# Kernel optimization log

Measured on AMD Instinct MI355X. Metric: run time of the kernel, lower is better.

## Reference

```python
import jax, jax.numpy as jnp
import numpy as np

B, S, D, H = 4, 2048, 1024, 16
DEPTH = D // H


def setup_inputs() -> dict:
    key = jax.random.key(0)
    ks = jax.random.split(key, 11)
    s = 1.0 / np.sqrt(D)
    return {
        "q": jax.random.normal(ks[0], (B, S, D), jnp.float32),
        "k": jax.random.normal(ks[1], (B, S, D), jnp.float32),
        "v": jax.random.normal(ks[2], (B, S, D), jnp.float32),
        "wq": jax.random.normal(ks[3], (D, D), jnp.float32) * s,
        "bq": jnp.zeros((D,), jnp.float32),
        "wk": jax.random.normal(ks[4], (D, D), jnp.float32) * s,
        "bk": jnp.zeros((D,), jnp.float32),
        "wv": jax.random.normal(ks[5], (D, D), jnp.float32) * s,
        "bv": jnp.zeros((D,), jnp.float32),
        "wo": jax.random.normal(ks[6], (D, D), jnp.float32) * s,
        "bo": jnp.zeros((D,), jnp.float32),
    }


def _split_heads(x):
    # [B,S,D] -> [B,H,S,depth]
    b, s, _ = x.shape
    return x.reshape(b, s, H, DEPTH).transpose(0, 2, 1, 3)


def reference(q, k, v, wq, bq, wk, bk, wv, bv, wo, bo):
    qh = _split_heads(q @ wq + bq)
    kh = _split_heads(k @ wk + bk)
    vh = _split_heads(v @ wv + bv)
    scale = 1.0 / jnp.sqrt(jnp.asarray(DEPTH, jnp.float32))
    logits = jnp.einsum("bhsd,bhtd->bhst", qh, kh) * scale  # [B,H,S,S]
    attn = jax.nn.softmax(logits, axis=-1)
    out = jnp.einsum("bhst,bhtd->bhsd", attn, vh)
    out = out.transpose(0, 2, 1, 3).reshape(q.shape[0], -1, D)
    return out @ wo + bo
```

## Files before the change

kernel.cpp:

```cpp
#include <hip/hip_runtime.h>
#include <hip/hip_bf16.h>

#define BATCH 4
#define SEQ   2048
#define DIM   1024
#define NHEAD 16
#define HDIM  64

typedef __bf16    bf16x8 __attribute__((ext_vector_type(8)));
typedef float     f32x16 __attribute__((ext_vector_type(16)));
typedef unsigned  u32;

__device__ __forceinline__ unsigned short f2bfu(float x) {
  union { __hip_bfloat16 b; unsigned short u; } c; c.b = __float2bfloat16(x); return c.u;
}
__device__ __forceinline__ u32 cvtpk(float lo, float hi) {
  u32 r; asm("v_cvt_pk_bf16_f32 %0, %1, %2" : "=v"(r) : "v"(lo), "v"(hi)); return r;
}
__device__ __forceinline__ int swz4(int row) {
  return ((row & 7) ^ ((row >> 3) & 7)) << 2;
}

#define GLDS16(GP, LP)                                                         \
  __builtin_amdgcn_global_load_lds(                                            \
      (const __attribute__((address_space(1))) void*)(GP),                     \
      (__attribute__((address_space(3))) void*)(LP), 16, 0, 0)

__global__ __launch_bounds__(256)
void wtrans(const float* __restrict__ w0, const float* __restrict__ w1,
            const float* __restrict__ w2,
            __hip_bfloat16* __restrict__ t0, __hip_bfloat16* __restrict__ t1,
            __hip_bfloat16* __restrict__ t2)
{
  __shared__ float T[64][68];
  const int mat  = blockIdx.x >> 8;
  const int tile = blockIdx.x & 255;
  const float* W = mat == 0 ? w0 : (mat == 1 ? w1 : w2);
  __hip_bfloat16* Wt = mat == 0 ? t0 : (mat == 1 ? t1 : t2);
  const int k0 = (tile >> 4) * 64, n0 = (tile & 15) * 64;
  const int tid = threadIdx.x;
  const int r = tid >> 2, cq = (tid & 3) * 16;
  #pragma unroll
  for (int j = 0; j < 4; ++j) {
    const float4 v = *reinterpret_cast<const float4*>(&W[(size_t)(k0 + r) * DIM + n0 + cq + j * 4]);
    T[r][cq + j * 4 + 0] = v.x; T[r][cq + j * 4 + 1] = v.y;
    T[r][cq + j * 4 + 2] = v.z; T[r][cq + j * 4 + 3] = v.w;
  }
  __syncthreads();
  u32 o[8];
  #pragma unroll
  for (int j = 0; j < 8; ++j)
    o[j] = cvtpk(T[cq + 2 * j][r], T[cq + 2 * j + 1][r]);
  *reinterpret_cast<uint4*>(&Wt[(size_t)(n0 + r) * DIM + k0 + cq + 0]) = make_uint4(o[0], o[1], o[2], o[3]);
  *reinterpret_cast<uint4*>(&Wt[(size_t)(n0 + r) * DIM + k0 + cq + 8]) = make_uint4(o[4], o[5], o[6], o[7]);
}

template<typename TIN, typename TOUT, int NSEG>
__global__ __launch_bounds__(256, 2)
void gemm1ph(const TIN* __restrict__ A0, const TIN* __restrict__ A1, const TIN* __restrict__ A2,
             const __hip_bfloat16* __restrict__ W0, const __hip_bfloat16* __restrict__ W1,
             const __hip_bfloat16* __restrict__ W2,
             const float* __restrict__ b0, const float* __restrict__ b1, const float* __restrict__ b2,
             TOUT* __restrict__ C0, TOUT* __restrict__ C1, TOUT* __restrict__ C2)
{
  __shared__ __align__(16) u32 As32[128][32];
  __shared__ __align__(16) u32 Bs32[128][32];

  constexpr bool AF32 = (sizeof(TIN) == 4);
  constexpr int K = 1024, NT = 16;

  const int seg = (NSEG == 1) ? 0 : (blockIdx.x >> 9);
  const int idb = (NSEG == 1) ? blockIdx.x : (blockIdx.x & 511);
  const TIN* A = seg == 0 ? A0 : (seg == 1 ? A1 : A2);
  const __hip_bfloat16* Wt = seg == 0 ? W0 : (seg == 1 ? W1 : W2);
  const float* bias = seg == 0 ? b0 : (seg == 1 ? b1 : b2);
  TOUT* C = seg == 0 ? C0 : (seg == 1 ? C1 : C2);

  const int xcd = idb & 7, rr = idb >> 3;
  const int bx = rr & 7, by = xcd + 8 * (rr >> 3);
  const int m0 = by * 128, n0 = bx * 128;

  const int tid = threadIdx.x, lane = tid & 63, w = tid >> 6;
  const int l31 = lane & 31, hi = lane >> 5;
  const int wm = w >> 1, wn = w & 1;

  f32x16 acc[2][2] = {};

  const __hip_bfloat16* bptr[4];
  #pragma unroll
  for (int i = 0; i < 4; ++i) {
    const int off = (w * 4 + i) * 1024 + lane * 16;
    const int r = off >> 7;
    const int s = (off >> 4) & 7;
    bptr[i] = Wt + (size_t)(n0 + r) * K + (s ^ (r & 7)) * 8;
  }
  const TIN* aptr[4];
  const int arow = tid >> 3;
  const int acb  = (tid & 7) * 8;
  #pragma unroll
  for (int i = 0; i < 4; ++i) {
    if constexpr (!AF32) {
      const int off = (w * 4 + i) * 1024 + lane * 16;
      const int r = off >> 7;
      const int s = (off >> 4) & 7;
      aptr[i] = A + (size_t)(m0 + r) * K + (s ^ (r & 7)) * 8;
    } else {
      aptr[i] = nullptr;
    }
  }

  float4 ar[4][2];

  auto loadA_f32 = [&](int t) {
    #pragma unroll
    for (int p = 0; p < 4; ++p) {
      const float* ap = (const float*)A + (size_t)(m0 + arow + p * 32) * K + t * 64 + acb;
      ar[p][0] = *reinterpret_cast<const float4*>(ap);
      ar[p][1] = *reinterpret_cast<const float4*>(ap + 4);
    }
  };
  auto writeA_f32 = [&]() {
    #pragma unroll
    for (int p = 0; p < 4; ++p) {
      const int row = arow + p * 32;
      uint4 pk;
      pk.x = cvtpk(ar[p][0].x, ar[p][0].y);
      pk.y = cvtpk(ar[p][0].z, ar[p][0].w);
      pk.z = cvtpk(ar[p][1].x, ar[p][1].y);
      pk.w = cvtpk(ar[p][1].z, ar[p][1].w);
      *reinterpret_cast<uint4*>(&As32[row][((tid & 7) * 4) ^ ((row & 7) << 2)]) = pk;
    }
  };
  auto stageA_bf = [&](int t) {
    #pragma unroll
    for (int i = 0; i < 4; ++i)
      GLDS16((const __hip_bfloat16*)aptr[i] + t * 64, (char*)As32 + (w * 4 + i) * 1024);
  };
  auto stageB = [&](int t) {
    #pragma unroll
    for (int i = 0; i < 4; ++i)
      GLDS16(bptr[i] + t * 64, (char*)Bs32 + (w * 4 + i) * 1024);
  };

  int aoff[4][2], boff[4][2];
  #pragma unroll
  for (int kk = 0; kk < 4; ++kk) {
    #pragma unroll
    for (int mi = 0; mi < 2; ++mi) {
      const int r = wm * 64 + mi * 32 + l31;
      aoff[kk][mi] = r * 128 + (((kk * 2 + hi) ^ (r & 7)) << 4);
    }
    #pragma unroll
    for (int ni = 0; ni < 2; ++ni) {
      const int c = wn * 64 + ni * 32 + l31;
      boff[kk][ni] = c * 128 + (((kk * 2 + hi) ^ (c & 7)) << 4);
    }
  }

  if constexpr (AF32) { loadA_f32(0); writeA_f32(); }
  else                { stageA_bf(0); }
  stageB(0);
  __syncthreads();

  for (int t = 0; t < NT; ++t) {
    if (t + 1 < NT) { if constexpr (AF32) loadA_f32(t + 1); }

    #pragma unroll
    for (int kk = 0; kk < 4; ++kk) {
      bf16x8 af[2], bfv[2];
      #pragma unroll
      for (int mi = 0; mi < 2; ++mi)
        af[mi] = *reinterpret_cast<const bf16x8*>((const char*)As32 + aoff[kk][mi]);
      #pragma unroll
      for (int ni = 0; ni < 2; ++ni)
        bfv[ni] = *reinterpret_cast<const bf16x8*>((const char*)Bs32 + boff[kk][ni]);
      __builtin_amdgcn_s_setprio(1);
      #pragma unroll
      for (int mi = 0; mi < 2; ++mi)
        #pragma unroll
        for (int ni = 0; ni < 2; ++ni)
          acc[mi][ni] = __builtin_amdgcn_mfma_f32_32x32x16_bf16(af[mi], bfv[ni], acc[mi][ni], 0, 0, 0);
      __builtin_amdgcn_s_setprio(0);
    }
    __syncthreads();

    if (t + 1 < NT) {
      if constexpr (AF32) writeA_f32();
      else                stageA_bf(t + 1);
      stageB(t + 1);
      __syncthreads();
    }
  }

  #pragma unroll
  for (int ni = 0; ni < 2; ++ni) {
    const int col = n0 + wn * 64 + ni * 32 + l31;
    const float bv = bias[col];
    #pragma unroll
    for (int mi = 0; mi < 2; ++mi) {
      #pragma unroll
      for (int g = 0; g < 4; ++g)
        #pragma unroll
        for (int e = 0; e < 4; ++e) {
          const int row = m0 + wm * 64 + mi * 32 + g * 8 + hi * 4 + e;
          const float val = acc[mi][ni][g * 4 + e] + bv;
          if constexpr (sizeof(TOUT) == 2)
            C[(size_t)row * DIM + col] = __float2bfloat16(val);
          else
            C[(size_t)row * DIM + col] = val;
        }
    }
  }
}

__global__ __launch_bounds__(256, 2)
void flash_attn(const __hip_bfloat16* __restrict__ Qb,
                const __hip_bfloat16* __restrict__ Kb,
                const __hip_bfloat16* __restrict__ Vb,
                __hip_bfloat16* __restrict__ Ob)
{
  __shared__ __align__(16) u32 Ks32[2][64][32];
  __shared__ __align__(16) u32 Vt32[2][64][32];

  const int id  = blockIdx.x;
  const int xcd = id & 7;
  const int r_  = id >> 3;
  const int qb  = r_ & 7;
  const int hh  = (r_ >> 3) & 1;
  const int b   = r_ >> 4;
  const int h   = xcd + 8 * hh;

  const int tid = threadIdx.x, lane = tid & 63, wv = tid >> 6;
  const int l31 = lane & 31, hi = lane >> 5;

  const size_t headoff = (size_t)h * HDIM;
  const int q0 = b * SEQ + qb * 256 + wv * 64;

  bf16x8 qf[2][4];
  #pragma unroll
  for (int qh = 0; qh < 2; ++qh)
    #pragma unroll
    for (int dk = 0; dk < 4; ++dk)
      qf[qh][dk] = *reinterpret_cast<const bf16x8*>(
        &Qb[(size_t)(q0 + qh * 32 + l31) * DIM + headoff + dk * 16 + hi * 8]);

  f32x16 accO[2][2] = {};
  float l_run[2] = {0.f, 0.f};

  const int skey = tid >> 2;
  const int sdq  = tid & 3;
  const int vkp  = tid >> 3;
  const int vdb  = tid & 7;
  const size_t kbase = (size_t)b * SEQ * DIM + headoff;

  uint4 kst[2], vst[2];
  auto load_t = [&](int t) {
    const int kb = t * 64;
    const __hip_bfloat16* kp_ = &Kb[kbase + (size_t)(kb + skey) * DIM + sdq * 16];
    kst[0] = *reinterpret_cast<const uint4*>(kp_);
    kst[1] = *reinterpret_cast<const uint4*>(kp_ + 8);
    const __hip_bfloat16* vp_ = &Vb[kbase + (size_t)(kb + vkp * 2) * DIM + vdb * 8];
    vst[0] = *reinterpret_cast<const uint4*>(vp_);
    vst[1] = *reinterpret_cast<const uint4*>(vp_ + DIM);
  };
  auto store_t = [&](int bb) {
    const int sk = swz4(skey);
    *reinterpret_cast<uint4*>(&Ks32[bb][skey][(sdq * 8 + 0) ^ sk]) = kst[0];
    *reinterpret_cast<uint4*>(&Ks32[bb][skey][(sdq * 8 + 4) ^ sk]) = kst[1];
    const unsigned short* a  = (const unsigned short*)&vst[0];
    const unsigned short* bv = (const unsigned short*)&vst[1];
    #pragma unroll
    for (int j = 0; j < 8; ++j) {
      const int row = vdb * 8 + j;
      Vt32[bb][row][vkp ^ swz4(row)] = (u32)a[j] | ((u32)bv[j] << 16);
    }
  };

  load_t(0); store_t(0); __syncthreads();

  const float C1 = 0.125f * 1.44269504f;

  for (int t = 0; t < SEQ / 64; ++t) {
    const int bb = t & 1;
    if (t < SEQ / 64 - 1) load_t(t + 1);

    f32x16 sacc[2][2] = {};
    __builtin_amdgcn_s_setprio(1);
    #pragma unroll
    for (int kt = 0; kt < 2; ++kt) {
      const int row = kt * 32 + l31;
      const int sk = swz4(row);
      #pragma unroll
      for (int dk = 0; dk < 4; ++dk) {
        bf16x8 kf = *reinterpret_cast<const bf16x8*>(&Ks32[bb][row][(dk * 8 + hi * 4) ^ sk]);
        sacc[0][kt] = __builtin_amdgcn_mfma_f32_32x32x16_bf16(kf, qf[0][dk], sacc[0][kt], 0, 0, 0);
        sacc[1][kt] = __builtin_amdgcn_mfma_f32_32x32x16_bf16(kf, qf[1][dk], sacc[1][kt], 0, 0, 0);
      }
    }
    __builtin_amdgcn_s_setprio(0);

    u32 pf[2][4][4];
    #pragma unroll
    for (int qh = 0; qh < 2; ++qh) {
      #pragma unroll
      for (int kt = 0; kt < 2; ++kt)
        #pragma unroll
        for (int r2 = 0; r2 < 16; ++r2)
          sacc[qh][kt][r2] = __builtin_amdgcn_exp2f(sacc[qh][kt][r2] * C1);

      f32x16 ps = sacc[qh][0] + sacc[qh][1];
      float s8[8];
      #pragma unroll
      for (int i = 0; i < 8; ++i) s8[i] = ps[i] + ps[i + 8];
      float rs = ((s8[0] + s8[1]) + (s8[2] + s8[3])) + ((s8[4] + s8[5]) + (s8[6] + s8[7]));
      rs += __shfl_xor(rs, 32);
      l_run[qh] += rs;

#define MAKE_PF(DST, P, B) do {                                            \
      u32 x1 = cvtpk(P[B+0], P[B+1]);                                      \
      u32 y1 = cvtpk(P[B+4], P[B+5]);                                      \
      u32 x2 = cvtpk(P[B+2], P[B+3]);                                      \
      u32 y2 = cvtpk(P[B+6], P[B+7]);                                      \
      auto s1 = __builtin_amdgcn_permlane32_swap(x1, y1, false, false);    \
      auto s2 = __builtin_amdgcn_permlane32_swap(x2, y2, false, false);    \
      DST[0] = (u32)s1[0]; DST[1] = (u32)s2[0];                            \
      DST[2] = (u32)s1[1]; DST[3] = (u32)s2[1];                            \
    } while (0)
      MAKE_PF(pf[qh][0], sacc[qh][0], 0);
      MAKE_PF(pf[qh][1], sacc[qh][0], 8);
      MAKE_PF(pf[qh][2], sacc[qh][1], 0);
      MAKE_PF(pf[qh][3], sacc[qh][1], 8);
#undef MAKE_PF
    }

    __builtin_amdgcn_s_setprio(1);
    #pragma unroll
    for (int dt = 0; dt < 2; ++dt) {
      const int row = dt * 32 + l31;
      const int sk = swz4(row);
      #pragma unroll
      for (int kf = 0; kf < 4; ++kf) {
        bf16x8 vf = *reinterpret_cast<const bf16x8*>(&Vt32[bb][row][(kf * 8 + hi * 4) ^ sk]);
        #pragma unroll
        for (int qh = 0; qh < 2; ++qh) {
          union { u32 u[4]; bf16x8 v; } pu;
          pu.u[0] = pf[qh][kf][0]; pu.u[1] = pf[qh][kf][1];
          pu.u[2] = pf[qh][kf][2]; pu.u[3] = pf[qh][kf][3];
          accO[qh][dt] = __builtin_amdgcn_mfma_f32_32x32x16_bf16(vf, pu.v, accO[qh][dt], 0, 0, 0);
        }
      }
    }
    __builtin_amdgcn_s_setprio(0);

    if (t < SEQ / 64 - 1) store_t(bb ^ 1);
    __syncthreads();
  }

  #pragma unroll
  for (int qh = 0; qh < 2; ++qh) {
    const float inv = 1.f / l_run[qh];
    const size_t rowbase = (size_t)(q0 + qh * 32 + l31) * DIM + headoff;
    #pragma unroll
    for (int dt = 0; dt < 2; ++dt)
      #pragma unroll
      for (int g = 0; g < 4; ++g) {
        ushort4 o;
        o.x = f2bfu(accO[qh][dt][g * 4 + 0] * inv);
        o.y = f2bfu(accO[qh][dt][g * 4 + 1] * inv);
        o.z = f2bfu(accO[qh][dt][g * 4 + 2] * inv);
        o.w = f2bfu(accO[qh][dt][g * 4 + 3] * inv);
        *reinterpret_cast<ushort4*>(&Ob[rowbase + dt * 32 + g * 8 + hi * 4]) = o;
      }
  }
}

extern "C" void kernel_launch(void* const* d_in, const int* in_sizes, int n_in,
                              void* d_out, int out_size, void* d_ws, size_t ws_size,
                              hipStream_t stream)
{
  const float* q  = (const float*)d_in[0];
  const float* k  = (const float*)d_in[1];
  const float* v  = (const float*)d_in[2];
  const float* wq = (const float*)d_in[3];
  const float* bq = (const float*)d_in[4];
  const float* wk = (const float*)d_in[5];
  const float* bk = (const float*)d_in[6];
  const float* wv = (const float*)d_in[7];
  const float* bv = (const float*)d_in[8];
  const float* wo = (const float*)d_in[9];
  const float* bo = (const float*)d_in[10];

  const size_t MN = (size_t)BATCH * SEQ * DIM;
  const size_t KK = (size_t)DIM * DIM;

  __hip_bfloat16* Qb = (__hip_bfloat16*)d_ws;
  __hip_bfloat16* Kb = Qb + MN;
  __hip_bfloat16* Vb = Kb + MN;
  __hip_bfloat16* S3 = Vb + MN;
  __hip_bfloat16* WtQ = S3;
  __hip_bfloat16* WtK = S3 + KK;
  __hip_bfloat16* WtV = S3 + 2 * KK;
  __hip_bfloat16* Ob  = S3;
  __hip_bfloat16* WtO = (__hip_bfloat16*)d_ws;

  wtrans<<<768, 256, 0, stream>>>(wq, wk, wv, WtQ, WtK, WtV);

  gemm1ph<float, __hip_bfloat16, 3><<<1536, 256, 0, stream>>>(
      q, k, v, WtQ, WtK, WtV, bq, bk, bv, Qb, Kb, Vb);

  flash_attn<<<512, 256, 0, stream>>>(Qb, Kb, Vb, Ob);

  wtrans<<<256, 256, 0, stream>>>(wo, wo, wo, WtO, WtO, WtO);

  gemm1ph<__hip_bfloat16, float, 1><<<512, 256, 0, stream>>>(
      Ob, Ob, Ob, WtO, WtO, WtO, bo, bo, bo,
      (float*)d_out, (float*)d_out, (float*)d_out);
}
```

Before: 200.8 us.

## Split flash attention into 8 waves of 32 query rows, fold softmax scale into Q projection

Flash attention now runs 512 threads per block, and each wave handles 32 query rows instead of 64. This halves per-wave accumulator and P registers and doubles the waves available for latency hiding. The K/V tile loads are split across more threads. The softmax scale (1/sqrt(d)·log2e) moves into the Q projection GEMM epilogue, removing a multiply per logit. As a trade-off, each K/V tile in LDS now feeds one MFMA per wave rather than two, which lowers arithmetic intensity per LDS read and raises LDS traffic.

```diff
diff --git a/kernel.cpp b/kernel.cpp
--- a/kernel.cpp
+++ b/kernel.cpp
@@ -61,7 +61,8 @@
              const __hip_bfloat16* __restrict__ W0, const __hip_bfloat16* __restrict__ W1,
              const __hip_bfloat16* __restrict__ W2,
              const float* __restrict__ b0, const float* __restrict__ b1, const float* __restrict__ b2,
-             TOUT* __restrict__ C0, TOUT* __restrict__ C1, TOUT* __restrict__ C2)
+             TOUT* __restrict__ C0, TOUT* __restrict__ C1, TOUT* __restrict__ C2,
+             float s0, float s1, float s2)
 {
   __shared__ __align__(16) u32 As32[128][32];
   __shared__ __align__(16) u32 Bs32[128][32];
@@ -75,6 +76,7 @@
   const __hip_bfloat16* Wt = seg == 0 ? W0 : (seg == 1 ? W1 : W2);
   const float* bias = seg == 0 ? b0 : (seg == 1 ? b1 : b2);
   TOUT* C = seg == 0 ? C0 : (seg == 1 ? C1 : C2);
+  const float scl = seg == 0 ? s0 : (seg == 1 ? s1 : s2);
 
   const int xcd = idb & 7, rr = idb >> 3;
   const int bx = rr & 7, by = xcd + 8 * (rr >> 3);
@@ -203,7 +205,7 @@
         #pragma unroll
         for (int e = 0; e < 4; ++e) {
           const int row = m0 + wm * 64 + mi * 32 + g * 8 + hi * 4 + e;
-          const float val = acc[mi][ni][g * 4 + e] + bv;
+          const float val = (acc[mi][ni][g * 4 + e] + bv) * scl;
           if constexpr (sizeof(TOUT) == 2)
             C[(size_t)row * DIM + col] = __float2bfloat16(val);
           else
@@ -213,7 +215,7 @@
   }
 }
 
-__global__ __launch_bounds__(256, 2)
+__global__ __launch_bounds__(512, 4)
 void flash_attn(const __hip_bfloat16* __restrict__ Qb,
                 const __hip_bfloat16* __restrict__ Kb,
                 const __hip_bfloat16* __restrict__ Vb,
@@ -230,61 +232,54 @@
   const int b   = r_ >> 4;
   const int h   = xcd + 8 * hh;
 
-  const int tid = threadIdx.x, lane = tid & 63, wv = tid >> 6;
+  const int tid = threadIdx.x, lane = tid & 63, w = tid >> 6;
   const int l31 = lane & 31, hi = lane >> 5;
 
   const size_t headoff = (size_t)h * HDIM;
-  const int q0 = b * SEQ + qb * 256 + wv * 64;
-
-  bf16x8 qf[2][4];
-  #pragma unroll
-  for (int qh = 0; qh < 2; ++qh)
-    #pragma unroll
-    for (int dk = 0; dk < 4; ++dk)
-      qf[qh][dk] = *reinterpret_cast<const bf16x8*>(
-        &Qb[(size_t)(q0 + qh * 32 + l31) * DIM + headoff + dk * 16 + hi * 8]);
-
-  f32x16 accO[2][2] = {};
-  float l_run[2] = {0.f, 0.f};
-
-  const int skey = tid >> 2;
-  const int sdq  = tid & 3;
-  const int vkp  = tid >> 3;
-  const int vdb  = tid & 7;
+  const int qrow = b * SEQ + qb * 256 + w * 32 + l31;
+
+  bf16x8 qf[4];
+  #pragma unroll
+  for (int dk = 0; dk < 4; ++dk)
+    qf[dk] = *reinterpret_cast<const bf16x8*>(
+      &Qb[(size_t)qrow * DIM + headoff + dk * 16 + hi * 8]);
+
+  f32x16 accO[2] = {};
+  float l_run = 0.f;
+
+  const int skey = tid >> 3;
+  const int sdq  = tid & 7;
+  const int vkp  = tid >> 4;
+  const int vdq  = tid & 15;
   const size_t kbase = (size_t)b * SEQ * DIM + headoff;
 
-  uint4 kst[2], vst[2];
+  uint4 kst;
+  uint2 vst0, vst1;
   auto load_t = [&](int t) {
     const int kb = t * 64;
-    const __hip_bfloat16* kp_ = &Kb[kbase + (size_t)(kb + skey) * DIM + sdq * 16];
-    kst[0] = *reinterpret_cast<const uint4*>(kp_);
-    kst[1] = *reinterpret_cast<const uint4*>(kp_ + 8);
-    const __hip_bfloat16* vp_ = &Vb[kbase + (size_t)(kb + vkp * 2) * DIM + vdb * 8];
-    vst[0] = *reinterpret_cast<const uint4*>(vp_);
-    vst[1] = *reinterpret_cast<const uint4*>(vp_ + DIM);
+    kst = *reinterpret_cast<const uint4*>(&Kb[kbase + (size_t)(kb + skey) * DIM + sdq * 8]);
+    const __hip_bfloat16* vp_ = &Vb[kbase + (size_t)(kb + vkp * 2) * DIM + vdq * 4];
+    vst0 = *reinterpret_cast<const uint2*>(vp_);
+    vst1 = *reinterpret_cast<const uint2*>(vp_ + DIM);
   };
   auto store_t = [&](int bb) {
-    const int sk = swz4(skey);
-    *reinterpret_cast<uint4*>(&Ks32[bb][skey][(sdq * 8 + 0) ^ sk]) = kst[0];
-    *reinterpret_cast<uint4*>(&Ks32[bb][skey][(sdq * 8 + 4) ^ sk]) = kst[1];
-    const unsigned short* a  = (const unsigned short*)&vst[0];
-    const unsigned short* bv = (const unsigned short*)&vst[1];
-    #pragma unroll
-    for (int j = 0; j < 8; ++j) {
-      const int row = vdb * 8 + j;
+    *reinterpret_cast<uint4*>(&Ks32[bb][skey][(sdq * 4) ^ swz4(skey)]) = kst;
+    const unsigned short* a  = (const unsigned short*)&vst0;
+    const unsigned short* bv = (const unsigned short*)&vst1;
+    #pragma unroll
+    for (int j = 0; j < 4; ++j) {
+      const int row = vdq * 4 + j;
       Vt32[bb][row][vkp ^ swz4(row)] = (u32)a[j] | ((u32)bv[j] << 16);
     }
   };
 
   load_t(0); store_t(0); __syncthreads();
-
-  const float C1 = 0.125f * 1.44269504f;
 
   for (int t = 0; t < SEQ / 64; ++t) {
     const int bb = t & 1;
     if (t < SEQ / 64 - 1) load_t(t + 1);
 
-    f32x16 sacc[2][2] = {};
+    f32x16 sacc[2] = {};
     __builtin_amdgcn_s_setprio(1);
     #pragma unroll
     for (int kt = 0; kt < 2; ++kt) {
@@ -293,45 +288,41 @@
       #pragma unroll
       for (int dk = 0; dk < 4; ++dk) {
         bf16x8 kf = *reinterpret_cast<const bf16x8*>(&Ks32[bb][row][(dk * 8 + hi * 4) ^ sk]);
-        sacc[0][kt] = __builtin_amdgcn_mfma_f32_32x32x16_bf16(kf, qf[0][dk], sacc[0][kt], 0, 0, 0);
-        sacc[1][kt] = __builtin_amdgcn_mfma_f32_32x32x16_bf16(kf, qf[1][dk], sacc[1][kt], 0, 0, 0);
+        sacc[kt] = __builtin_amdgcn_mfma_f32_32x32x16_bf16(kf, qf[dk], sacc[kt], 0, 0, 0);
       }
     }
     __builtin_amdgcn_s_setprio(0);
 
-    u32 pf[2][4][4];
-    #pragma unroll
-    for (int qh = 0; qh < 2; ++qh) {
-      #pragma unroll
-      for (int kt = 0; kt < 2; ++kt)
-        #pragma unroll
-        for (int r2 = 0; r2 < 16; ++r2)
-          sacc[qh][kt][r2] = __builtin_amdgcn_exp2f(sacc[qh][kt][r2] * C1);
-
-      f32x16 ps = sacc[qh][0] + sacc[qh][1];
-      float s8[8];
-      #pragma unroll
-      for (int i = 0; i < 8; ++i) s8[i] = ps[i] + ps[i + 8];
-      float rs = ((s8[0] + s8[1]) + (s8[2] + s8[3])) + ((s8[4] + s8[5]) + (s8[6] + s8[7]));
-      rs += __shfl_xor(rs, 32);
-      l_run[qh] += rs;
-
+    #pragma unroll
+    for (int kt = 0; kt < 2; ++kt)
+      #pragma unroll
+      for (int r2 = 0; r2 < 16; ++r2)
+        sacc[kt][r2] = __builtin_amdgcn_exp2f(sacc[kt][r2]);
+
+    f32x16 ps = sacc[0] + sacc[1];
+    float s8[8];
+    #pragma unroll
+    for (int i = 0; i < 8; ++i) s8[i] = ps[i] + ps[i + 8];
+    float rs = ((s8[0] + s8[1]) + (s8[2] + s8[3])) + ((s8[4] + s8[5]) + (s8[6] + s8[7]));
+    rs += __shfl_xor(rs, 32);
+    l_run += rs;
+
+    u32 pf[4][4];
 #define MAKE_PF(DST, P, B) do {                                            \
       u32 x1 = cvtpk(P[B+0], P[B+1]);                                      \
       u32 y1 = cvtpk(P[B+4], P[B+5]);                                      \
       u32 x2 = cvtpk(P[B+2], P[B+3]);                                      \
       u32 y2 = cvtpk(P[B+6], P[B+7]);                                      \
-      auto s1 = __builtin_amdgcn_permlane32_swap(x1, y1, false, false);    \
-      auto s2 = __builtin_amdgcn_permlane32_swap(x2, y2, false, false);    \
-      DST[0] = (u32)s1[0]; DST[1] = (u32)s2[0];                            \
-      DST[2] = (u32)s1[1]; DST[3] = (u32)s2[1];                            \
+      auto s1_ = __builtin_amdgcn_permlane32_swap(x1, y1, false, false);   \
+      auto s2_ = __builtin_amdgcn_permlane32_swap(x2, y2, false, false);   \
+      DST[0] = (u32)s1_[0]; DST[1] = (u32)s2_[0];                          \
+      DST[2] = (u32)s1_[1]; DST[3] = (u32)s2_[1];                          \
     } while (0)
-      MAKE_PF(pf[qh][0], sacc[qh][0], 0);
-      MAKE_PF(pf[qh][1], sacc[qh][0], 8);
-      MAKE_PF(pf[qh][2], sacc[qh][1], 0);
-      MAKE_PF(pf[qh][3], sacc[qh][1], 8);
+    MAKE_PF(pf[0], sacc[0], 0);
+    MAKE_PF(pf[1], sacc[0], 8);
+    MAKE_PF(pf[2], sacc[1], 0);
+    MAKE_PF(pf[3], sacc[1], 8);
 #undef MAKE_PF
-    }
 
     __builtin_amdgcn_s_setprio(1);
     #pragma unroll
@@ -341,13 +332,10 @@
       #pragma unroll
       for (int kf = 0; kf < 4; ++kf) {
         bf16x8 vf = *reinterpret_cast<const bf16x8*>(&Vt32[bb][row][(kf * 8 + hi * 4) ^ sk]);
-        #pragma unroll
-        for (int qh = 0; qh < 2; ++qh) {
-          union { u32 u[4]; bf16x8 v; } pu;
-          pu.u[0] = pf[qh][kf][0]; pu.u[1] = pf[qh][kf][1];
-          pu.u[2] = pf[qh][kf][2]; pu.u[3] = pf[qh][kf][3];
-          accO[qh][dt] = __builtin_amdgcn_mfma_f32_32x32x16_bf16(vf, pu.v, accO[qh][dt], 0, 0, 0);
-        }
+        union { u32 u[4]; bf16x8 v; } pu;
+        pu.u[0] = pf[kf][0]; pu.u[1] = pf[kf][1];
+        pu.u[2] = pf[kf][2]; pu.u[3] = pf[kf][3];
+        accO[dt] = __builtin_amdgcn_mfma_f32_32x32x16_bf16(vf, pu.v, accO[dt], 0, 0, 0);
       }
     }
     __builtin_amdgcn_s_setprio(0);
@@ -356,22 +344,19 @@
     __syncthreads();
   }
 
-  #pragma unroll
-  for (int qh = 0; qh < 2; ++qh) {
-    const float inv = 1.f / l_run[qh];
-    const size_t rowbase = (size_t)(q0 + qh * 32 + l31) * DIM + headoff;
-    #pragma unroll
-    for (int dt = 0; dt < 2; ++dt)
-      #pragma unroll
-      for (int g = 0; g < 4; ++g) {
-        ushort4 o;
-        o.x = f2bfu(accO[qh][dt][g * 4 + 0] * inv);
-        o.y = f2bfu(accO[qh][dt][g * 4 + 1] * inv);
-        o.z = f2bfu(accO[qh][dt][g * 4 + 2] * inv);
-        o.w = f2bfu(accO[qh][dt][g * 4 + 3] * inv);
-        *reinterpret_cast<ushort4*>(&Ob[rowbase + dt * 32 + g * 8 + hi * 4]) = o;
-      }
-  }
+  const float inv = 1.f / l_run;
+  const size_t rowbase = (size_t)qrow * DIM + headoff;
+  #pragma unroll
+  for (int dt = 0; dt < 2; ++dt)
+    #pragma unroll
+    for (int g = 0; g < 4; ++g) {
+      ushort4 o;
+      o.x = f2bfu(accO[dt][g * 4 + 0] * inv);
+      o.y = f2bfu(accO[dt][g * 4 + 1] * inv);
+      o.z = f2bfu(accO[dt][g * 4 + 2] * inv);
+      o.w = f2bfu(accO[dt][g * 4 + 3] * inv);
+      *reinterpret_cast<ushort4*>(&Ob[rowbase + dt * 32 + g * 8 + hi * 4]) = o;
+    }
 }
 
 extern "C" void kernel_launch(void* const* d_in, const int* in_sizes, int n_in,
@@ -392,6 +377,7 @@
 
   const size_t MN = (size_t)BATCH * SEQ * DIM;
   const size_t KK = (size_t)DIM * DIM;
+  const float  C1 = 0.125f * 1.44269504f;
 
   __hip_bfloat16* Qb = (__hip_bfloat16*)d_ws;
   __hip_bfloat16* Kb = Qb + MN;
@@ -406,13 +392,13 @@
   wtrans<<<768, 256, 0, stream>>>(wq, wk, wv, WtQ, WtK, WtV);
 
   gemm1ph<float, __hip_bfloat16, 3><<<1536, 256, 0, stream>>>(
-      q, k, v, WtQ, WtK, WtV, bq, bk, bv, Qb, Kb, Vb);
-
-  flash_attn<<<512, 256, 0, stream>>>(Qb, Kb, Vb, Ob);
+      q, k, v, WtQ, WtK, WtV, bq, bk, bv, Qb, Kb, Vb, C1, 1.0f, 1.0f);
+
+  flash_attn<<<512, 512, 0, stream>>>(Qb, Kb, Vb, Ob);
 
   wtrans<<<256, 256, 0, stream>>>(wo, wo, wo, WtO, WtO, WtO);
 
   gemm1ph<__hip_bfloat16, float, 1><<<512, 256, 0, stream>>>(
       Ob, Ob, Ob, WtO, WtO, WtO, bo, bo, bo,
-      (float*)d_out, (float*)d_out, (float*)d_out);
-}
+      (float*)d_out, (float*)d_out, (float*)d_out, 1.0f, 1.0f, 1.0f);
+}
```

Result: slower. 206.6 us (+2.9%).
